# Kernel optimization log

Measured on AMD Instinct MI355X. Metric: run time of the kernel, lower is better.

## Reference

```python
import jax, jax.numpy as jnp
import numpy as np

B, C, H, W_IMG = 4, 4, 512, 512
OUT_CH = 256
POS_NUM = 512
NEG_NUM = 512
M_MARGIN = 0.5
TAU = 0.1
EPS = 1e-8


def setup_inputs() -> dict:
    key = jax.random.key(0)
    k1, k2, k3, k4, k5, k6 = jax.random.split(key, 6)
    d1_fegc = jax.random.normal(k1, (B, C, H, W_IMG), dtype=jnp.float32)
    p_fegc = jax.random.uniform(k2, (B, 1, H, W_IMG), dtype=jnp.float32)
    p_pre = jax.random.uniform(k3, (B, 3, H, W_IMG), dtype=jnp.float32)
    gt = (jax.random.uniform(k4, (B, 1, H, W_IMG)) < 0.5).astype(jnp.float32)
    # parameters of the nn.Linear(in_channel, out_channel)
    W = jax.random.normal(k5, (OUT_CH, C), dtype=jnp.float32) / np.sqrt(C)
    b_fc = jax.random.normal(k6, (OUT_CH,), dtype=jnp.float32) * 0.01
    return {"d1_fegc": d1_fegc, "p_fegc": p_fegc, "p_pre": p_pre, "gt": gt, "W": W, "b_fc": b_fc}


def _sample_idx(mask_flat, key, n):
    # randomized fixed-size sampling of n indices where mask is True
    # (replaces torch.nonzero + randperm with a jit-friendly top-k over random scores)
    score = jnp.where(mask_flat, jax.random.uniform(key, mask_flat.shape), -jnp.inf)
    _, idx = jax.lax.top_k(score, n)
    return idx


def reference(d1_fegc, p_fegc, p_pre, gt, W, b_fc):
    b, c, h, w = d1_fegc.shape
    P = POS_NUM * b
    N = NEG_NUM * b
    # p_overlap channel 3: fegc foreground AND pre argmax-class 0
    fegc_fg = p_fegc[:, 0] >= 0.5                       # [b,h,w]
    pre_cls0 = jnp.argmax(p_pre, axis=1) == 0           # [b,h,w]
    pre_region = fegc_fg & pre_cls0                     # [b,h,w]
    gt_fg = gt[:, 0] > 0.5                              # [b,h,w]
    pos_mask = (pre_region & gt_fg).reshape(-1)         # [b*h*w]
    neg_mask = (pre_region & ~gt_fg).reshape(-1)        # [b*h*w]
    # per-pixel feature vectors from d1_fegc
    feats = d1_fegc.transpose(0, 2, 3, 1).reshape(-1, c)  # [b*h*w, c]
    skey = jax.random.key(42)
    kp, kn = jax.random.split(skey)
    pos_idx = _sample_idx(pos_mask, kp, P)
    neg_idx = _sample_idx(neg_mask, kn, N)
    pts = jnp.concatenate([feats[pos_idx], feats[neg_idx]], axis=0)  # [P+N, c]
    proj = pts @ W.T + b_fc                                           # [P+N, out]
    # F.cosine_similarity with eps=1e-8 norm clamping
    norm = jnp.maximum(jnp.linalg.norm(proj, axis=-1, keepdims=True), EPS)
    normed = proj / norm
    cos_sim = normed @ normed.T                                       # [P+N, P+N]
    T = P + N
    label = jnp.ones((T, T), dtype=cos_sim.dtype)
    label = label.at[:P, P:].set(0.0).at[P:, :P].set(0.0)
    s = cos_sim / TAU
    lam = (1.0 - label) * jnp.square(s) + label * jnp.square(jnp.maximum(M_MARGIN - s, 0.0))
    lam = lam * (1.0 - jnp.eye(T, dtype=lam.dtype))                   # mask self pairs
    denom = jnp.sum(lam != 0).astype(lam.dtype)
    return jnp.sum(lam) / denom
```

## Files before the change

### kernel.cpp

```cpp
#include <hip/hip_runtime.h>
#include <stdint.h>

#define HW       262144u
#define NPIX     1048576u
#define NSEL     2048u
#define NSEG     1024u
#define SEGCAP   16u
#define DENSECAP 3584u
#define NTILE    32u
#define NPBLK    528u

#define OFF_SEG   0u
#define OFF_IDX   262144u
#define OFF_VA    278528u
#define OFF_WA    360448u
#define OFF_PSUM  442368u
#define OFF_PNNZ  446464u
#define OFF_G     450560u

#define TF_ROUND(r) { x0 += x1; x1 = (x1 << (r)) | (x1 >> (32 - (r))); x1 ^= x0; }
__host__ __device__ inline void threefry2x32_(uint32_t k0, uint32_t k1,
                                              uint32_t& x0, uint32_t& x1) {
  uint32_t k2 = k0 ^ k1 ^ 0x1BD11BDAu;
  x0 += k0; x1 += k1;
  TF_ROUND(13) TF_ROUND(15) TF_ROUND(26) TF_ROUND(6)
  x0 += k1; x1 += k2 + 1u;
  TF_ROUND(17) TF_ROUND(29) TF_ROUND(16) TF_ROUND(24)
  x0 += k2; x1 += k0 + 2u;
  TF_ROUND(13) TF_ROUND(15) TF_ROUND(26) TF_ROUND(6)
  x0 += k0; x1 += k1 + 3u;
  TF_ROUND(17) TF_ROUND(29) TF_ROUND(16) TF_ROUND(24)
  x0 += k1; x1 += k2 + 4u;
  TF_ROUND(13) TF_ROUND(15) TF_ROUND(26) TF_ROUND(6)
  x0 += k2; x1 += k0 + 5u;
}

__global__ __launch_bounds__(256) void k_front(
    const float* __restrict__ pfegc, const float* __restrict__ ppre,
    const float* __restrict__ gt, const float* __restrict__ Wm,
    const float* __restrict__ bfc,
    uint32_t kp0, uint32_t kp1, uint32_t kn0, uint32_t kn1,
    uint64_t* __restrict__ seg, float* __restrict__ Gout) {
  __shared__ uint32_t cnt2[2];
  __shared__ float sGw[4][25];
  int t = threadIdx.x;
  uint32_t b = blockIdx.x;
  if (t < 2) cnt2[t] = 0;
  if (t < 2 * (int)SEGCAP) {
    uint32_t list = (uint32_t)t / SEGCAP, slot = (uint32_t)t % SEGCAP;
    seg[((size_t)list * NSEG + b) * SEGCAP + slot] = 0ull;
  }
  __syncthreads();
  uint32_t base = b * 1024u + (uint32_t)t * 4u;
  float4 pf = *(const float4*)(pfegc + base);
  float pfa[4] = { pf.x, pf.y, pf.z, pf.w };
  bool any = (pf.x >= 0.5f) || (pf.y >= 0.5f) || (pf.z >= 0.5f) || (pf.w >= 0.5f);
  if (any) {
    uint32_t hw = base & (HW - 1u);
    uint32_t bb = base >> 18;
    const float* pp = ppre + (size_t)bb * 3u * HW + hw;
    float4 p0 = *(const float4*)pp;
    float4 p1 = *(const float4*)(pp + HW);
    float4 p2 = *(const float4*)(pp + 2u * HW);
    float p0a[4] = { p0.x, p0.y, p0.z, p0.w };
    float p1a[4] = { p1.x, p1.y, p1.z, p1.w };
    float p2a[4] = { p2.x, p2.y, p2.z, p2.w };
    bool c[4]; bool anyc = false;
    #pragma unroll
    for (int j = 0; j < 4; ++j) {
      c[j] = (pfa[j] >= 0.5f) && (p0a[j] >= p1a[j]) && (p0a[j] >= p2a[j]);
      anyc |= c[j];
    }
    if (anyc) {
      float4 g4 = *(const float4*)(gt + base);
      float ga[4] = { g4.x, g4.y, g4.z, g4.w };
      #pragma unroll
      for (int j = 0; j < 4; ++j) {
        if (c[j]) {
          uint32_t i = base + (uint32_t)j;
          bool gfg = ga[j] > 0.5f;
          uint32_t x0 = 0u, x1 = i;
          threefry2x32_(gfg ? kp0 : kn0, gfg ? kp1 : kn1, x0, x1);
          uint32_t r23 = (x0 ^ x1) >> 9;
          if ((r23 >> 18) == 0x1Fu) {
            uint32_t list = gfg ? 0u : 1u;
            uint32_t r = atomicAdd(&cnt2[list], 1u);
            if (r < SEGCAP)
              seg[((size_t)list * NSEG + b) * SEGCAP + r] =
                  (1ull << 43) | ((uint64_t)r23 << 20) | (uint64_t)(0xFFFFFu ^ i);
          }
        }
      }
    }
  }
  if (b == 0) {
    float4 wr = *(const float4*)(Wm + t * 4);
    float av[5] = { wr.x, wr.y, wr.z, wr.w, bfc[t] };
    int lane = t & 63, wvi = t >> 6;
    #pragma unroll
    for (int p = 0; p < 5; ++p)
      #pragma unroll
      for (int q = p; q < 5; ++q) {
        float g = av[p] * av[q];
        #pragma unroll
        for (int off = 32; off > 0; off >>= 1)
          g += __shfl_xor(g, off, 64);
        if (lane == 0) sGw[wvi][p * 5 + q] = g;
      }
    __syncthreads();
    if (t < 25) {
      int p = t / 5, q = t % 5;
      int pp = p < q ? p : q, qq = p < q ? q : p;
      Gout[t] = sGw[0][pp * 5 + qq] + sGw[1][pp * 5 + qq]
              + sGw[2][pp * 5 + qq] + sGw[3][pp * 5 + qq];
    }
  }
}

__global__ __launch_bounds__(1024) void k_sel(
    const uint64_t* __restrict__ seg, uint32_t* __restrict__ idxbuf) {
  __shared__ uint64_t dense[DENSECAP];
  __shared__ uint32_t hist[8192];
  __shared__ uint64_t bnd[128];
  __shared__ uint32_t wsum[16];
  __shared__ uint32_t dcnt, bcnt, rank, sb, sneed;
  __shared__ uint64_t sthr;
  int t = threadIdx.x;
  int list = blockIdx.x;
  uint32_t lane = (uint32_t)t & 63u, wv = (uint32_t)t >> 6;
  if (t == 0) { dcnt = 0u; bcnt = 0u; rank = 0u; sb = 0u; sneed = 1u; }
  #pragma unroll
  for (int e = 0; e < 8; ++e) hist[e * 1024 + t] = 0u;
  __syncthreads();
  const uint4* sp4 = (const uint4*)(seg + (size_t)list * NSEG * SEGCAP);
  #pragma unroll
  for (int it = 0; it < 8; ++it) {
    uint4 v = sp4[(uint32_t)it * 1024u + (uint32_t)t];
    uint64_t k0 = ((uint64_t)v.y << 32) | v.x;
    uint64_t k1 = ((uint64_t)v.w << 32) | v.z;
    #pragma unroll
    for (int h = 0; h < 2; ++h) {
      uint64_t k = h ? k1 : k0;
      bool val = (k >> 43) != 0ull;
      unsigned long long mb = __ballot(val);
      uint32_t bs = 0;
      if (lane == 0 && mb) bs = atomicAdd(&dcnt, (uint32_t)__popcll(mb));
      bs = (uint32_t)__shfl((int)bs, 0, 64);
      if (val) {
        uint32_t s2 = bs + (uint32_t)__popcll(mb & ((1ull << lane) - 1ull));
        if (s2 < DENSECAP) dense[s2] = k;
      }
    }
  }
  __syncthreads();
  uint32_t n = dcnt; if (n > DENSECAP) n = DENSECAP;
  for (uint32_t j = t; j < n; j += 1024)
    atomicAdd(&hist[(uint32_t)(dense[j] >> 25) & 8191u], 1u);
  __syncthreads();
  uint32_t s = 0;
  #pragma unroll
  for (int e = 0; e < 8; ++e) s += hist[t * 8 + e];
  uint32_t suf = s;
  #pragma unroll
  for (int off = 1; off < 64; off <<= 1) {
    uint32_t v = (uint32_t)__shfl_down((int)suf, off, 64);
    if (lane + (uint32_t)off < 64u) suf += v;
  }
  if (lane == 0) wsum[wv] = suf;
  __syncthreads();
  uint32_t wafter = 0;
  for (uint32_t u = wv + 1u; u < 16u; ++u) wafter += wsum[u];
  uint32_t after_t = wafter + (suf - s);
  if (after_t < NSEL && after_t + s >= NSEL) {
    uint32_t running = after_t;
    for (int e = 7; e >= 0; --e) {
      uint32_t h = hist[t * 8 + e];
      running += h;
      if (running >= NSEL) { sb = (uint32_t)(t * 8 + e); sneed = NSEL - (running - h); break; }
    }
  }
  __syncthreads();
  uint32_t b_star = sb, need = sneed;
  for (uint32_t j = t; j < n; j += 1024) {
    uint64_t k = dense[j];
    if (((uint32_t)(k >> 25) & 8191u) == b_star) {
      uint32_t p = atomicAdd(&bcnt, 1u);
      if (p < 128u) bnd[p] = k;
    }
  }
  __syncthreads();
  if (t == 0) {
    uint32_t m = bcnt; if (m > 128u) m = 128u;
    uint64_t thr = bnd[0];
    for (uint32_t i = 0; i < m; ++i) {
      uint32_t rk = 1u;
      for (uint32_t j = 0; j < m; ++j) rk += (bnd[j] > bnd[i]) ? 1u : 0u;
      if (rk == need) { thr = bnd[i]; break; }
    }
    sthr = thr;
  }
  __syncthreads();
  uint64_t thr = sthr;
  uint32_t niter = (n + 1023u) >> 10;
  for (uint32_t it2 = 0; it2 < niter; ++it2) {
    uint32_t j = it2 * 1024u + (uint32_t)t;
    uint64_t k = 0ull;
    bool v = false;
    if (j < n) { k = dense[j]; v = (k >= thr); }
    unsigned long long mb = __ballot(v);
    uint32_t bs = 0;
    if (lane == 0 && mb) bs = atomicAdd(&rank, (uint32_t)__popcll(mb));
    bs = (uint32_t)__shfl((int)bs, 0, 64);
    if (v) {
      uint32_t s2 = bs + (uint32_t)__popcll(mb & ((1ull << lane) - 1ull));
      if (s2 < NSEL)
        idxbuf[(uint32_t)list * NSEL + s2] = 0xFFFFFu ^ (uint32_t)(k & 0xFFFFFu);
    }
  }
}

__global__ __launch_bounds__(64) void k_proj(
    const uint32_t* __restrict__ idxbuf, const float* __restrict__ Gin,
    const float* __restrict__ d1,
    float* __restrict__ va, float* __restrict__ wa) {
  __shared__ float sG[25];
  int t = threadIdx.x;
  if (t < 25) sG[t] = Gin[t];
  __syncthreads();
  uint32_t tg = blockIdx.x * 64u + (uint32_t)t;
  uint32_t idx = idxbuf[tg] & (NPIX - 1u);
  uint32_t hw = idx & (HW - 1u);
  uint32_t bb = idx >> 18;
  const float* f = d1 + ((size_t)bb << 20) + hw;
  float y[5] = { f[0], f[HW], f[2u * HW], f[3u * HW], 1.0f };
  float z[5]; float n2 = 0.f;
  #pragma unroll
  for (int p = 0; p < 5; ++p) {
    float acc = 0.f;
    #pragma unroll
    for (int q = 0; q < 5; ++q) acc += sG[p * 5 + q] * y[q];
    z[p] = acc; n2 += acc * y[p];
  }
  n2 = fmaxf(n2, 0.f);
  float inv = 1.0f / fmaxf(sqrtf(n2), 1e-8f);
  uint32_t s5 = tg * 5u;
  #pragma unroll
  for (int p = 0; p < 5; ++p) {
    va[s5 + p] = y[p] * inv;
    wa[s5 + p] = z[p] * inv;
  }
}

__global__ __launch_bounds__(256) void k_pair(
    const float* __restrict__ va, const float* __restrict__ wa,
    float* __restrict__ psum, uint32_t* __restrict__ pnnz) {
  __shared__ __align__(16) float sv[640], sw[640];
  __shared__ float wps[4];
  __shared__ uint32_t wpn[4];
  uint32_t bi = 0, rem = blockIdx.x;
  while (rem >= (NTILE - bi)) { rem -= (NTILE - bi); ++bi; }
  uint32_t bj = bi + rem;
  int i0 = (int)bi * 128, j0 = (int)bj * 128;
  int t = threadIdx.x;
  int lane = t & 63, wv = t >> 6;
  if (t < 160) {
    ((float4*)sv)[t] = ((const float4*)(va + i0 * 5))[t];
    ((float4*)sw)[t] = ((const float4*)(wa + j0 * 5))[t];
  }
  __syncthreads();
  int ty = t >> 4, tx = t & 15;
  float rv[8][5], rw[8][5];
  #pragma unroll
  for (int a = 0; a < 8; ++a)
    #pragma unroll
    for (int p = 0; p < 5; ++p) {
      rv[a][p] = sv[(ty * 8 + a) * 5 + p];
      rw[a][p] = sw[(tx * 8 + a) * 5 + p];
    }
  float lsum = 0.f; uint32_t lnz = 0;
  #pragma unroll
  for (int a = 0; a < 8; ++a) {
    int gi = i0 + ty * 8 + a;
    #pragma unroll
    for (int q = 0; q < 8; ++q) {
      int gj = j0 + tx * 8 + q;
      float c = rv[a][0]*rw[q][0] + rv[a][1]*rw[q][1] + rv[a][2]*rw[q][2]
              + rv[a][3]*rw[q][3] + rv[a][4]*rw[q][4];
      float sc = c * 10.0f;
      if (gi < gj) {
        if (((gi ^ gj) & 2048) == 0) {
          float m = fmaxf(0.5f - sc, 0.f);
          lsum += m * m;
          lnz += (m > 0.f) ? 1u : 0u;
        } else {
          lsum += sc * sc;
          lnz += (sc != 0.f) ? 1u : 0u;
        }
      }
    }
  }
  #pragma unroll
  for (int off = 32; off > 0; off >>= 1) {
    lsum += __shfl_xor(lsum, off, 64);
    lnz  += (uint32_t)__shfl_xor((int)lnz, off, 64);
  }
  if (lane == 0) { wps[wv] = lsum; wpn[wv] = lnz; }
  __syncthreads();
  if (t == 0) {
    psum[blockIdx.x] = wps[0] + wps[1] + wps[2] + wps[3];
    pnnz[blockIdx.x] = wpn[0] + wpn[1] + wpn[2] + wpn[3];
  }
}

__global__ __launch_bounds__(256) void k_final(const float* __restrict__ psum,
                                               const uint32_t* __restrict__ pnnz,
                                               float* __restrict__ out) {
  __shared__ float wps[4];
  __shared__ uint32_t wpn[4];
  int t = threadIdx.x;
  int lane = t & 63, wv = t >> 6;
  float s = 0.f; uint32_t nz = 0u;
  for (int j = t; j < (int)NPBLK; j += 256) { s += psum[j]; nz += pnnz[j]; }
  #pragma unroll
  for (int off = 32; off > 0; off >>= 1) {
    s  += __shfl_xor(s, off, 64);
    nz += (uint32_t)__shfl_xor((int)nz, off, 64);
  }
  if (lane == 0) { wps[wv] = s; wpn[wv] = nz; }
  __syncthreads();
  if (t == 0)
    out[0] = (wps[0] + wps[1] + wps[2] + wps[3])
           / (float)(wpn[0] + wpn[1] + wpn[2] + wpn[3]);
}

extern "C" void kernel_launch(void* const* d_in, const int* in_sizes, int n_in,
                              void* d_out, int out_size, void* d_ws, size_t ws_size,
                              hipStream_t stream) {
  (void)in_sizes; (void)n_in; (void)out_size; (void)ws_size;
  const float* d1    = (const float*)d_in[0];
  const float* pfegc = (const float*)d_in[1];
  const float* ppre  = (const float*)d_in[2];
  const float* gt    = (const float*)d_in[3];
  const float* W     = (const float*)d_in[4];
  const float* bfc   = (const float*)d_in[5];
  float* out = (float*)d_out;

  uint8_t* base = (uint8_t*)d_ws;
  uint64_t* seg    = (uint64_t*)(base + OFF_SEG);
  uint32_t* idxbuf = (uint32_t*)(base + OFF_IDX);
  float*    va     = (float*)(base + OFF_VA);
  float*    wa     = (float*)(base + OFF_WA);
  float*    psum   = (float*)(base + OFF_PSUM);
  uint32_t* pnnz   = (uint32_t*)(base + OFF_PNNZ);
  float*    Gws    = (float*)(base + OFF_G);

  uint32_t kp0 = 0u, kp1 = 0u; threefry2x32_(0u, 42u, kp0, kp1);
  uint32_t kn0 = 0u, kn1 = 1u; threefry2x32_(0u, 42u, kn0, kn1);

  k_front<<<NSEG, 256, 0, stream>>>(pfegc, ppre, gt, W, bfc,
                                    kp0, kp1, kn0, kn1, seg, Gws);
  k_sel<<<2, 1024, 0, stream>>>(seg, idxbuf);
  k_proj<<<64, 64, 0, stream>>>(idxbuf, Gws, d1, va, wa);
  k_pair<<<NPBLK, 256, 0, stream>>>(va, wa, psum, pnnz);
  k_final<<<1, 256, 0, stream>>>(psum, pnnz, out);
}
```

Before: 105.9 us.

## Fuse projection into pair kernel and load front inputs unconditionally

Removes the separate k_proj launch. Each k_pair block now gathers its 256 sampled pixels from d1, applies the Gram-matrix projection and normalisation, and writes the results straight into shared memory instead of staging them through global va/wa buffers. This saves one kernel launch and a global round-trip, at the cost of redundant projection work across the 528 pair blocks and scattered d1 gathers in every block. In k_front, the ppre and gt loads are hoisted out of the data-dependent branches so all loads are issued together, trading extra memory traffic for fewer serialized dependent loads.

```diff
diff --git a/kernel.cpp b/kernel.cpp
--- a/kernel.cpp
+++ b/kernel.cpp
@@ -12,11 +12,9 @@
 
 #define OFF_SEG   0u
 #define OFF_IDX   262144u
-#define OFF_VA    278528u
-#define OFF_WA    360448u
-#define OFF_PSUM  442368u
-#define OFF_PNNZ  446464u
-#define OFF_G     450560u
+#define OFF_PSUM  278528u
+#define OFF_PNNZ  282624u
+#define OFF_G     286720u
 
 #define TF_ROUND(r) { x0 += x1; x1 = (x1 << (r)) | (x1 >> (32 - (r))); x1 ^= x0; }
 __host__ __device__ inline void threefry2x32_(uint32_t k0, uint32_t k1,
@@ -52,44 +50,33 @@
   }
   __syncthreads();
   uint32_t base = b * 1024u + (uint32_t)t * 4u;
+  uint32_t hw = base & (HW - 1u);
+  uint32_t bb = base >> 18;
+  const float* pp = ppre + (size_t)bb * 3u * HW + hw;
   float4 pf = *(const float4*)(pfegc + base);
+  float4 p0 = *(const float4*)pp;
+  float4 p1 = *(const float4*)(pp + HW);
+  float4 p2 = *(const float4*)(pp + 2u * HW);
+  float4 g4 = *(const float4*)(gt + base);
   float pfa[4] = { pf.x, pf.y, pf.z, pf.w };
-  bool any = (pf.x >= 0.5f) || (pf.y >= 0.5f) || (pf.z >= 0.5f) || (pf.w >= 0.5f);
-  if (any) {
-    uint32_t hw = base & (HW - 1u);
-    uint32_t bb = base >> 18;
-    const float* pp = ppre + (size_t)bb * 3u * HW + hw;
-    float4 p0 = *(const float4*)pp;
-    float4 p1 = *(const float4*)(pp + HW);
-    float4 p2 = *(const float4*)(pp + 2u * HW);
-    float p0a[4] = { p0.x, p0.y, p0.z, p0.w };
-    float p1a[4] = { p1.x, p1.y, p1.z, p1.w };
-    float p2a[4] = { p2.x, p2.y, p2.z, p2.w };
-    bool c[4]; bool anyc = false;
-    #pragma unroll
-    for (int j = 0; j < 4; ++j) {
-      c[j] = (pfa[j] >= 0.5f) && (p0a[j] >= p1a[j]) && (p0a[j] >= p2a[j]);
-      anyc |= c[j];
-    }
-    if (anyc) {
-      float4 g4 = *(const float4*)(gt + base);
-      float ga[4] = { g4.x, g4.y, g4.z, g4.w };
-      #pragma unroll
-      for (int j = 0; j < 4; ++j) {
-        if (c[j]) {
-          uint32_t i = base + (uint32_t)j;
-          bool gfg = ga[j] > 0.5f;
-          uint32_t x0 = 0u, x1 = i;
-          threefry2x32_(gfg ? kp0 : kn0, gfg ? kp1 : kn1, x0, x1);
-          uint32_t r23 = (x0 ^ x1) >> 9;
-          if ((r23 >> 18) == 0x1Fu) {
-            uint32_t list = gfg ? 0u : 1u;
-            uint32_t r = atomicAdd(&cnt2[list], 1u);
-            if (r < SEGCAP)
-              seg[((size_t)list * NSEG + b) * SEGCAP + r] =
-                  (1ull << 43) | ((uint64_t)r23 << 20) | (uint64_t)(0xFFFFFu ^ i);
-          }
-        }
+  float p0a[4] = { p0.x, p0.y, p0.z, p0.w };
+  float p1a[4] = { p1.x, p1.y, p1.z, p1.w };
+  float p2a[4] = { p2.x, p2.y, p2.z, p2.w };
+  float ga[4]  = { g4.x, g4.y, g4.z, g4.w };
+  #pragma unroll
+  for (int j = 0; j < 4; ++j) {
+    if (pfa[j] >= 0.5f && p0a[j] >= p1a[j] && p0a[j] >= p2a[j]) {
+      uint32_t i = base + (uint32_t)j;
+      bool gfg = ga[j] > 0.5f;
+      uint32_t x0 = 0u, x1 = i;
+      threefry2x32_(gfg ? kp0 : kn0, gfg ? kp1 : kn1, x0, x1);
+      uint32_t r23 = (x0 ^ x1) >> 9;
+      if ((r23 >> 18) == 0x1Fu) {
+        uint32_t list = gfg ? 0u : 1u;
+        uint32_t r = atomicAdd(&cnt2[list], 1u);
+        if (r < SEGCAP)
+          seg[((size_t)list * NSEG + b) * SEGCAP + r] =
+              (1ull << 43) | ((uint64_t)r23 << 20) | (uint64_t)(0xFFFFFu ^ i);
       }
     }
   }
@@ -110,9 +97,9 @@
     __syncthreads();
     if (t < 25) {
       int p = t / 5, q = t % 5;
-      int pp = p < q ? p : q, qq = p < q ? q : p;
-      Gout[t] = sGw[0][pp * 5 + qq] + sGw[1][pp * 5 + qq]
-              + sGw[2][pp * 5 + qq] + sGw[3][pp * 5 + qq];
+      int pp2 = p < q ? p : q, qq = p < q ? q : p;
+      Gout[t] = sGw[0][pp2 * 5 + qq] + sGw[1][pp2 * 5 + qq]
+              + sGw[2][pp2 * 5 + qq] + sGw[3][pp2 * 5 + qq];
     }
   }
 }
@@ -219,42 +206,12 @@
   }
 }
 
-__global__ __launch_bounds__(64) void k_proj(
+__global__ __launch_bounds__(256) void k_pair(
     const uint32_t* __restrict__ idxbuf, const float* __restrict__ Gin,
     const float* __restrict__ d1,
-    float* __restrict__ va, float* __restrict__ wa) {
-  __shared__ float sG[25];
-  int t = threadIdx.x;
-  if (t < 25) sG[t] = Gin[t];
-  __syncthreads();
-  uint32_t tg = blockIdx.x * 64u + (uint32_t)t;
-  uint32_t idx = idxbuf[tg] & (NPIX - 1u);
-  uint32_t hw = idx & (HW - 1u);
-  uint32_t bb = idx >> 18;
-  const float* f = d1 + ((size_t)bb << 20) + hw;
-  float y[5] = { f[0], f[HW], f[2u * HW], f[3u * HW], 1.0f };
-  float z[5]; float n2 = 0.f;
-  #pragma unroll
-  for (int p = 0; p < 5; ++p) {
-    float acc = 0.f;
-    #pragma unroll
-    for (int q = 0; q < 5; ++q) acc += sG[p * 5 + q] * y[q];
-    z[p] = acc; n2 += acc * y[p];
-  }
-  n2 = fmaxf(n2, 0.f);
-  float inv = 1.0f / fmaxf(sqrtf(n2), 1e-8f);
-  uint32_t s5 = tg * 5u;
-  #pragma unroll
-  for (int p = 0; p < 5; ++p) {
-    va[s5 + p] = y[p] * inv;
-    wa[s5 + p] = z[p] * inv;
-  }
-}
-
-__global__ __launch_bounds__(256) void k_pair(
-    const float* __restrict__ va, const float* __restrict__ wa,
     float* __restrict__ psum, uint32_t* __restrict__ pnnz) {
   __shared__ __align__(16) float sv[640], sw[640];
+  __shared__ float sG[25];
   __shared__ float wps[4];
   __shared__ uint32_t wpn[4];
   uint32_t bi = 0, rem = blockIdx.x;
@@ -263,9 +220,30 @@
   int i0 = (int)bi * 128, j0 = (int)bj * 128;
   int t = threadIdx.x;
   int lane = t & 63, wv = t >> 6;
-  if (t < 160) {
-    ((float4*)sv)[t] = ((const float4*)(va + i0 * 5))[t];
-    ((float4*)sw)[t] = ((const float4*)(wa + j0 * 5))[t];
+  if (t < 25) sG[t] = Gin[t];
+  uint32_t pt = (t < 128) ? (uint32_t)(i0 + t) : (uint32_t)(j0 + t - 128);
+  uint32_t idx = idxbuf[pt] & (NPIX - 1u);
+  uint32_t hw = idx & (HW - 1u);
+  uint32_t bb = idx >> 18;
+  const float* f = d1 + ((size_t)bb << 20) + hw;
+  float y[5] = { f[0], f[HW], f[2u * HW], f[3u * HW], 1.0f };
+  __syncthreads();
+  float z[5]; float n2 = 0.f;
+  #pragma unroll
+  for (int p = 0; p < 5; ++p) {
+    float acc = 0.f;
+    #pragma unroll
+    for (int q = 0; q < 5; ++q) acc += sG[p * 5 + q] * y[q];
+    z[p] = acc; n2 += acc * y[p];
+  }
+  n2 = fmaxf(n2, 0.f);
+  float inv = 1.0f / fmaxf(sqrtf(n2), 1e-8f);
+  if (t < 128) {
+    #pragma unroll
+    for (int p = 0; p < 5; ++p) sv[t * 5 + p] = y[p] * inv;
+  } else {
+    #pragma unroll
+    for (int p = 0; p < 5; ++p) sw[(t - 128) * 5 + p] = z[p] * inv;
   }
   __syncthreads();
   int ty = t >> 4, tx = t & 15;
@@ -348,8 +326,6 @@
   uint8_t* base = (uint8_t*)d_ws;
   uint64_t* seg    = (uint64_t*)(base + OFF_SEG);
   uint32_t* idxbuf = (uint32_t*)(base + OFF_IDX);
-  float*    va     = (float*)(base + OFF_VA);
-  float*    wa     = (float*)(base + OFF_WA);
   float*    psum   = (float*)(base + OFF_PSUM);
   uint32_t* pnnz   = (uint32_t*)(base + OFF_PNNZ);
   float*    Gws    = (float*)(base + OFF_G);
@@ -360,7 +336,6 @@
   k_front<<<NSEG, 256, 0, stream>>>(pfegc, ppre, gt, W, bfc,
                                     kp0, kp1, kn0, kn1, seg, Gws);
   k_sel<<<2, 1024, 0, stream>>>(seg, idxbuf);
-  k_proj<<<64, 64, 0, stream>>>(idxbuf, Gws, d1, va, wa);
-  k_pair<<<NPBLK, 256, 0, stream>>>(va, wa, psum, pnnz);
+  k_pair<<<NPBLK, 256, 0, stream>>>(idxbuf, Gws, d1, psum, pnnz);
   k_final<<<1, 256, 0, stream>>>(psum, pnnz, out);
 }
```

After: 109.2 us. +3.1%, slower.
